# Optimization experiments

Hardware: AMD Instinct MI355X
Metric: run time of the kernel (lower is better)

## Reference

```python
import jax, jax.numpy as jnp
import numpy as np

N = 100000   # nodes
E = 1600000  # edges
G = 512      # graphs in batch
F_IN = 128
H = 128
F_OUT = 1


def setup_inputs() -> dict:
    key = jax.random.key(0)
    ks = jax.random.split(key, 12)
    x = jax.random.normal(ks[0], (N, F_IN), dtype=jnp.float32)
    src = jax.random.randint(ks[1], (E,), 0, N, dtype=jnp.int32)
    dst = jax.random.randint(ks[2], (E,), 0, N, dtype=jnp.int32)
    node2graph = jnp.sort(jax.random.randint(ks[3], (N,), 0, G, dtype=jnp.int32))
    s_in = 1.0 / np.sqrt(F_IN)
    s_h = 1.0 / np.sqrt(H)
    W0 = jax.random.normal(ks[4], (F_IN, H), dtype=jnp.float32) * s_in
    b0 = jnp.zeros((H,), dtype=jnp.float32)
    W1 = jax.random.normal(ks[5], (H, H), dtype=jnp.float32) * s_h
    b1 = jnp.zeros((H,), dtype=jnp.float32)
    W2 = jax.random.normal(ks[6], (H, H), dtype=jnp.float32) * s_h
    b2 = jnp.zeros((H,), dtype=jnp.float32)
    Wm1 = jax.random.normal(ks[7], (H, H), dtype=jnp.float32) * s_h
    bm1 = jnp.zeros((H,), dtype=jnp.float32)
    Wm2 = jax.random.normal(ks[8], (H, F_OUT), dtype=jnp.float32) * s_h
    bm2 = jnp.zeros((F_OUT,), dtype=jnp.float32)
    return {"x": x, "src": src, "dst": dst, "node2graph": node2graph,
            "W0": W0, "b0": b0, "W1": W1, "b1": b1, "W2": W2, "b2": b2,
            "Wm1": Wm1, "bm1": bm1, "Wm2": Wm2, "bm2": bm2}


def _degree_norms(src, dst):
    ones = jnp.ones((E,), dtype=jnp.float32)
    out_deg = jax.ops.segment_sum(ones, src, num_segments=N)
    in_deg = jax.ops.segment_sum(ones, dst, num_segments=N)
    norm_out = jax.lax.rsqrt(jnp.maximum(out_deg, 1.0))  # [N]
    norm_in = jax.lax.rsqrt(jnp.maximum(in_deg, 1.0))    # [N]
    return norm_out, norm_in


def _graph_conv(x, src, dst, norm_out, norm_in, W, b):
    # DGL GraphConv, norm='both', in_feats <= out_feats path:
    # aggregate normalized src features, then linear + activation.
    xs = x * norm_out[:, None]
    msg = xs[src]                                         # [E, H] gather
    agg = jax.ops.segment_sum(msg, dst, num_segments=N)   # [N, H] scatter-add
    agg = agg * norm_in[:, None]
    return jax.nn.relu(agg @ W + b)


def reference(x, src, dst, node2graph, W0, b0, W1, b1, W2, b2, Wm1, bm1, Wm2, bm2):
    norm_out, norm_in = _degree_norms(src, dst)
    h = _graph_conv(x, src, dst, norm_out, norm_in, W0, b0)
    h = _graph_conv(h, src, dst, norm_out, norm_in, W1, b1)
    h = _graph_conv(h, src, dst, norm_out, norm_in, W2, b2)
    # sum_nodes readout per graph
    g = jax.ops.segment_sum(h, node2graph, num_segments=G)  # [G, H]
    # MLP head: Linear -> ReLU -> Linear
    return jax.nn.relu(g @ Wm1 + bm1) @ Wm2 + bm2           # [G, 1]
```

## Files before the change

kernel.cpp:

```cpp
#include <hip/hip_runtime.h>

#define NN 100000
#define NE 1600000
#define NG 512
#define HD 128

#define NBK 196
#define CHUNK 6400
#define NC 250
#define LH (2 * NBK * NC)
#define BCAP 11264

typedef _Float16 h8 __attribute__((ext_vector_type(8)));
typedef float f32x4 __attribute__((ext_vector_type(4)));

__global__ __launch_bounds__(1024) void k_hist(const int* __restrict__ src,
                                               const int* __restrict__ dst,
                                               int* __restrict__ H,
                                               const float* __restrict__ W0,
                                               const float* __restrict__ W1,
                                               const float* __restrict__ W2,
                                               _Float16* __restrict__ Bt) {
    if (blockIdx.x >= NC) {
        int i = (blockIdx.x - NC) * 1024 + threadIdx.x;
        int w = i >> 14;
        int rem = i & 16383;
        int n = rem >> 7;
        int k = rem & 127;
        const float* W = (w == 0) ? W0 : ((w == 1) ? W1 : W2);
        Bt[i] = (_Float16)W[k * 128 + n];
        return;
    }
    __shared__ int hd[NBK], hs[NBK];
    int c = blockIdx.x;
    for (int i = threadIdx.x; i < NBK; i += 1024) { hd[i] = 0; hs[i] = 0; }
    __syncthreads();
    int e0 = c * CHUNK;
    int e1 = e0 + CHUNK; if (e1 > NE) e1 = NE;
    for (int e = e0 + threadIdx.x; e < e1; e += 1024) {
        atomicAdd(&hd[dst[e] >> 9], 1);
        atomicAdd(&hs[src[e] >> 9], 1);
    }
    __syncthreads();
    for (int i = threadIdx.x; i < NBK; i += 1024) {
        H[i * NC + c] = hd[i];
        H[NBK * NC + i * NC + c] = hs[i];
    }
}

__global__ __launch_bounds__(256) void k_scan1g(int* __restrict__ H,
                                                int* __restrict__ bsum, int L) {
    __shared__ int s[256];
    int i = blockIdx.x * 256 + threadIdx.x;
    int v = (i < L) ? H[i] : 0;
    s[threadIdx.x] = v;
    __syncthreads();
    for (int off = 1; off < 256; off <<= 1) {
        int t = (threadIdx.x >= off) ? s[threadIdx.x - off] : 0;
        __syncthreads();
        s[threadIdx.x] += t;
        __syncthreads();
    }
    if (i < L) H[i] = s[threadIdx.x] - v;
    if (threadIdx.x == 255) bsum[blockIdx.x] = s[255];
}

__global__ __launch_bounds__(256) void k_scan3g(int* __restrict__ H,
                                                const int* __restrict__ bsum,
                                                int L, int nb) {
    __shared__ int sb[512];
    __shared__ int tmp2[256];
    int t = threadIdx.x;
    int b0 = (2 * t < nb) ? bsum[2 * t] : 0;
    int b1 = (2 * t + 1 < nb) ? bsum[2 * t + 1] : 0;
    int pair = b0 + b1;
    tmp2[t] = pair;
    __syncthreads();
    for (int off = 1; off < 256; off <<= 1) {
        int v2 = (t >= off) ? tmp2[t - off] : 0;
        __syncthreads();
        tmp2[t] += v2;
        __syncthreads();
    }
    int ex = tmp2[t] - pair;
    sb[2 * t] = ex;
    sb[2 * t + 1] = ex + b0;
    __syncthreads();
    int i = blockIdx.x * 256 + t;
    if (i < L) H[i] += sb[i >> 8];
}

__global__ __launch_bounds__(1024) void k_scatter(const int* __restrict__ src,
                                                  const int* __restrict__ dst,
                                                  const int* __restrict__ H,
                                                  int* __restrict__ dpart,
                                                  unsigned short* __restrict__ spart) {
    __shared__ int valbuf[CHUNK];
    __shared__ unsigned short bidbuf[CHUNK];
    __shared__ int lcur[NBK], delta[NBK];
    __shared__ int tmp[256];
    int c = blockIdx.x;
    int t = threadIdx.x;
    int e0 = c * CHUNK;
    int e1 = e0 + CHUNK; if (e1 > NE) e1 = NE;
    int n = e1 - e0;

    {
        int v = 0;
        if (t < NBK) {
            int curp = H[t * NC + c];
            int nxtp = (c + 1 < NC) ? H[t * NC + c + 1]
                                    : ((t + 1 < NBK) ? H[(t + 1) * NC] : NE);
            v = nxtp - curp;
            delta[t] = curp;
        }
        if (t < 256) tmp[t] = v;
        __syncthreads();
        for (int off = 1; off < 256; off <<= 1) {
            int add = (t < 256 && t >= off) ? tmp[t - off] : 0;
            __syncthreads();
            if (t < 256) tmp[t] += add;
            __syncthreads();
        }
        if (t < NBK) {
            int lbase = tmp[t] - v;
            lcur[t] = lbase;
            delta[t] -= lbase;
        }
    }
    __syncthreads();
    for (int e = e0 + t; e < e1; e += 1024) {
        int s = src[e], d = dst[e];
        int b = d >> 9;
        int q = atomicAdd(&lcur[b], 1);
        valbuf[q] = s | ((d & 511) << 17);
        bidbuf[q] = (unsigned short)b;
    }
    __syncthreads();
    for (int i = t; i < n; i += 1024) dpart[delta[bidbuf[i]] + i] = valbuf[i];
    __syncthreads();

    {
        int v = 0;
        if (t < NBK) {
            int curp = H[NBK * NC + t * NC + c] - NE;
            int nxtp = (c + 1 < NC) ? H[NBK * NC + t * NC + c + 1] - NE
                                    : ((t + 1 < NBK) ? H[NBK * NC + (t + 1) * NC] - NE : NE);
            v = nxtp - curp;
            delta[t] = curp;
        }
        if (t < 256) tmp[t] = v;
        __syncthreads();
        for (int off = 1; off < 256; off <<= 1) {
            int add = (t < 256 && t >= off) ? tmp[t - off] : 0;
            __syncthreads();
            if (t < 256) tmp[t] += add;
            __syncthreads();
        }
        if (t < NBK) {
            int lbase = tmp[t] - v;
            lcur[t] = lbase;
            delta[t] -= lbase;
        }
    }
    __syncthreads();
    for (int e = e0 + t; e < e1; e += 1024) {
        int s = src[e];
        int b = s >> 9;
        int q = atomicAdd(&lcur[b], 1);
        valbuf[q] = s & 511;
        bidbuf[q] = (unsigned short)b;
    }
    __syncthreads();
    for (int i = t; i < n; i += 1024)
        spart[delta[bidbuf[i]] + i] = (unsigned short)valbuf[i];
}

__global__ __launch_bounds__(1024) void k_bucket(const int* __restrict__ dpart,
                                                 const unsigned short* __restrict__ spart,
                                                 const int* __restrict__ H,
                                                 int* __restrict__ offs,
                                                 int* __restrict__ csr,
                                                 float* __restrict__ ni,
                                                 float* __restrict__ no) {
    __shared__ int deg[512];
    __shared__ int lcur[512];
    __shared__ int tmp[1024];
    __shared__ int csrbuf[BCAP];
    int b = blockIdx.x;
    bool isDst = (b < NBK);
    int bb = isDst ? b : b - NBK;
    int start, end;
    if (isDst) {
        start = H[bb * NC];
        end = (bb + 1 < NBK) ? H[(bb + 1) * NC] : NE;
    } else {
        start = H[NBK * NC + bb * NC] - NE;
        end = (bb + 1 < NBK) ? H[NBK * NC + (bb + 1) * NC] - NE : NE;
    }
    int t = threadIdx.x;
    if (t < 512) deg[t] = 0;
    __syncthreads();
    if (isDst) {
        for (int i = start + t; i < end; i += 1024)
            atomicAdd(&deg[(dpart[i] >> 17) & 511], 1);
    } else {
        for (int i = start + t; i < end; i += 1024)
            atomicAdd(&deg[spart[i]], 1);
    }
    __syncthreads();
    int vb = bb * 512;
    if (!isDst) {
        if (t < 512) {
            int v = vb + t;
            if (v < NN) no[v] = rsqrtf(fmaxf((float)deg[t], 1.0f));
        }
        return;
    }
    int a = (t < 512) ? deg[t] : 0;
    tmp[t] = a;
    __syncthreads();
    for (int off = 1; off < 1024; off <<= 1) {
        int v2 = (t >= off) ? tmp[t - off] : 0;
        __syncthreads();
        tmp[t] += v2;
        __syncthreads();
    }
    if (t < 512) {
        lcur[t] = tmp[t] - a;
        int v = vb + t;
        if (v < NN) {
            offs[v] = start + lcur[t];
            ni[v] = rsqrtf(fmaxf((float)a, 1.0f));
        }
    }
    if (b == NBK - 1 && t == 0) offs[NN] = NE;
    __syncthreads();
    int len = end - start;
    bool fits = (len <= BCAP);
    for (int i = start + t; i < end; i += 1024) {
        int pk = dpart[i];
        int q = atomicAdd(&lcur[(pk >> 17) & 511], 1);
        if (fits) csrbuf[q] = pk & 0x1FFFF;
        else      csr[start + q] = pk & 0x1FFFF;
    }
    __syncthreads();
    if (fits) {
        for (int i = t; i < len; i += 1024) csr[start + i] = csrbuf[i];
    }
}

template <typename TA>
__global__ __launch_bounds__(256) void k_gemm_mfma(const TA* __restrict__ A,
                                                   const _Float16* __restrict__ Bt,
                                                   const float* __restrict__ no,
                                                   _Float16* __restrict__ Zh,
                                                   int nrows) {
    __shared__ _Float16 Bs[128 * 136];
    int tid = threadIdx.x;
    {
        const h8* B8 = (const h8*)Bt;
        h8* Bs8 = (h8*)Bs;
        for (int i = tid; i < 2048; i += 256) {
            int n = i >> 4, c = i & 15;
            Bs8[n * 17 + c] = B8[i];
        }
    }

    int wave = tid >> 6;
    int lane = tid & 63;
    int m16 = lane & 15;
    int quad = lane >> 4;
    int rowbase = blockIdx.x * 64 + wave * 16;
    int row = rowbase + m16;
    bool valid = row < nrows;

    h8 afrag[4];
    if (valid) {
        if constexpr (sizeof(TA) == 2) {
            const h8* Arow = (const h8*)(A + (size_t)row * 128);
#pragma unroll
            for (int kk = 0; kk < 4; kk++) afrag[kk] = Arow[kk * 4 + quad];
        } else {
            const float4* Arow = (const float4*)(A + (size_t)row * 128);
#pragma unroll
            for (int kk = 0; kk < 4; kk++) {
                float4 lo = Arow[kk * 8 + quad * 2];
                float4 hi = Arow[kk * 8 + quad * 2 + 1];
                h8 a;
                a[0] = (_Float16)lo.x; a[1] = (_Float16)lo.y;
                a[2] = (_Float16)lo.z; a[3] = (_Float16)lo.w;
                a[4] = (_Float16)hi.x; a[5] = (_Float16)hi.y;
                a[6] = (_Float16)hi.z; a[7] = (_Float16)hi.w;
                afrag[kk] = a;
            }
        }
    } else {
#pragma unroll
        for (int kk = 0; kk < 4; kk++) {
            h8 a;
#pragma unroll
            for (int j = 0; j < 8; j++) a[j] = (_Float16)0.f;
            afrag[kk] = a;
        }
    }

    __syncthreads();

    f32x4 acc[8];
#pragma unroll
    for (int nt = 0; nt < 8; nt++) acc[nt] = (f32x4){0.f, 0.f, 0.f, 0.f};

    const h8* Bs8 = (const h8*)Bs;
#pragma unroll
    for (int nt = 0; nt < 8; nt++) {
        const h8* Bp = Bs8 + (size_t)(nt * 16 + m16) * 17;
#pragma unroll
        for (int kk = 0; kk < 4; kk++) {
            acc[nt] = __builtin_amdgcn_mfma_f32_16x16x32_f16(afrag[kk], Bp[kk * 4 + quad],
                                                             acc[nt], 0, 0, 0);
        }
    }

    float nor[4];
#pragma unroll
    for (int r = 0; r < 4; r++) {
        int grow = rowbase + quad * 4 + r;
        nor[r] = (grow < nrows) ? no[grow] : 0.f;
    }

    __syncthreads();
    {
        int lr0 = wave * 16 + quad * 4;
#pragma unroll
        for (int nt = 0; nt < 8; nt++) {
#pragma unroll
            for (int r = 0; r < 4; r++) {
                Bs[(size_t)(lr0 + r) * 136 + nt * 16 + m16] =
                    (_Float16)(acc[nt][r] * nor[r]);
            }
        }
    }
    __syncthreads();

    int blockrow0 = blockIdx.x * 64;
    for (int i = tid; i < 1024; i += 256) {
        int r = i >> 4, cch = i & 15;
        int grow = blockrow0 + r;
        if (grow < nrows) {
            h8 val = *(const h8*)&Bs[(size_t)r * 136 + cch * 8];
            *(h8*)&Zh[(size_t)grow * 128 + cch * 8] = val;
        }
    }
}

__global__ __launch_bounds__(256) void k_agg(const h8* __restrict__ Zh,
                                             const int* __restrict__ offs,
                                             const int* __restrict__ csr,
                                             const float* __restrict__ ni,
                                             const float* __restrict__ b,
                                             h8* __restrict__ H16) {
    int v = blockIdx.x * 16 + (threadIdx.x >> 4);
    int c = threadIdx.x & 15;
    int s = offs[v];
    int e = offs[v + 1];
    float a0[8], a1[8];
#pragma unroll
    for (int j = 0; j < 8; j++) { a0[j] = 0.f; a1[j] = 0.f; }
    int i = s;
    for (; i + 4 <= e; i += 4) {
        int u0 = csr[i];
        int u1 = csr[i + 1];
        int u2 = csr[i + 2];
        int u3 = csr[i + 3];
        h8 z0 = Zh[(size_t)u0 * 16 + c];
        h8 z1 = Zh[(size_t)u1 * 16 + c];
        h8 z2 = Zh[(size_t)u2 * 16 + c];
        h8 z3 = Zh[(size_t)u3 * 16 + c];
#pragma unroll
        for (int j = 0; j < 8; j++) {
            a0[j] += (float)z0[j] + (float)z1[j];
            a1[j] += (float)z2[j] + (float)z3[j];
        }
    }
    for (; i < e; i++) {
        int u = csr[i];
        h8 z = Zh[(size_t)u * 16 + c];
#pragma unroll
        for (int j = 0; j < 8; j++) a0[j] += (float)z[j];
    }
    float niv = ni[v];
    const float* bb = b + c * 8;
    h8 r;
#pragma unroll
    for (int j = 0; j < 8; j++)
        r[j] = (_Float16)fmaxf((a0[j] + a1[j]) * niv + bb[j], 0.f);
    H16[(size_t)v * 16 + c] = r;
}

__global__ __launch_bounds__(256) void k_gsum(const h8* __restrict__ H8,
                                              const int* __restrict__ n2g,
                                              float* __restrict__ gbuf) {
    __shared__ float red[256 * 8];
    int gi = blockIdx.x >> 2;
    int part = blockIdx.x & 3;
    int t = threadIdx.x;
    int slot = t >> 4;
    int c = t & 15;

    int lo = 0, hi = NN;
    while (lo < hi) { int mid = (lo + hi) >> 1; if (n2g[mid] < gi) lo = mid + 1; else hi = mid; }
    int s = lo;
    hi = NN;
    while (lo < hi) { int mid = (lo + hi) >> 1; if (n2g[mid] < gi + 1) lo = mid + 1; else hi = mid; }
    int e = lo;

    float acc[8];
#pragma unroll
    for (int j = 0; j < 8; j++) acc[j] = 0.f;
    for (int v = s + part * 16 + slot; v < e; v += 64) {
        h8 z = H8[(size_t)v * 16 + c];
#pragma unroll
        for (int j = 0; j < 8; j++) acc[j] += (float)z[j];
    }
#pragma unroll
    for (int j = 0; j < 8; j++) red[t * 8 + j] = acc[j];
    __syncthreads();
    for (int off = 8; off >= 1; off >>= 1) {
        if (slot < off) {
#pragma unroll
            for (int j = 0; j < 8; j++)
                red[t * 8 + j] += red[(t + off * 16) * 8 + j];
        }
        __syncthreads();
    }
    if (slot == 0) {
#pragma unroll
        for (int j = 0; j < 8; j++)
            gbuf[((size_t)part * NG + gi) * 128 + c * 8 + j] = red[t * 8 + j];
    }
}

__global__ __launch_bounds__(128) void k_head(const float* __restrict__ gbuf,
                                              const float* __restrict__ Wm1,
                                              const float* __restrict__ bm1,
                                              const float* __restrict__ Wm2,
                                              const float* __restrict__ bm2,
                                              float* __restrict__ out) {
    __shared__ float gs[128];
    __shared__ float red2[128];
    int gi = blockIdx.x;
    int t = threadIdx.x;
    gs[t] = gbuf[(size_t)gi * 128 + t] +
            gbuf[((size_t)NG + gi) * 128 + t] +
            gbuf[((size_t)2 * NG + gi) * 128 + t] +
            gbuf[((size_t)3 * NG + gi) * 128 + t];
    __syncthreads();
    float a = bm1[t];
    for (int k = 0; k < 128; k++) a += gs[k] * Wm1[k * 128 + t];
    red2[t] = fmaxf(a, 0.f) * Wm2[t];
    __syncthreads();
    for (int s2 = 64; s2 > 0; s2 >>= 1) {
        if (t < s2) red2[t] += red2[t + s2];
        __syncthreads();
    }
    if (t == 0) out[gi] = red2[0] + bm2[0];
}

extern "C" void kernel_launch(void* const* d_in, const int* in_sizes, int n_in,
                              void* d_out, int out_size, void* d_ws, size_t ws_size,
                              hipStream_t stream) {
    const float* x   = (const float*)d_in[0];
    const int*   src = (const int*)d_in[1];
    const int*   dst = (const int*)d_in[2];
    const int*   n2g = (const int*)d_in[3];
    const float* W0  = (const float*)d_in[4];
    const float* b0  = (const float*)d_in[5];
    const float* W1  = (const float*)d_in[6];
    const float* b1  = (const float*)d_in[7];
    const float* W2  = (const float*)d_in[8];
    const float* b2  = (const float*)d_in[9];
    const float* Wm1 = (const float*)d_in[10];
    const float* bm1 = (const float*)d_in[11];
    const float* Wm2 = (const float*)d_in[12];
    const float* bm2 = (const float*)d_in[13];
    float* out = (float*)d_out;

    char* p = (char*)d_ws;
    auto carve = [&](size_t bytes) -> char* {
        char* r = p;
        p += (bytes + 255) & ~(size_t)255;
        return r;
    };
    _Float16* zh  = (_Float16*)carve((size_t)NN * HD * 2);
    _Float16* h16 = (_Float16*)carve((size_t)NN * HD * 2);
    _Float16* Bt  = (_Float16*)carve((size_t)3 * 128 * 128 * 2);
    float* no     = (float*)carve((size_t)NN * 4);
    float* ni     = (float*)carve((size_t)NN * 4);
    int*   offs   = (int*)carve((size_t)(NN + 1) * 4);
    int*   csr    = (int*)carve((size_t)NE * 4);
    int*   Hh     = (int*)carve((size_t)LH * 4);
    int*   bsum   = (int*)carve((size_t)512 * 4);
    int*   dpart  = (int*)carve((size_t)NE * 4);
    unsigned short* spart = (unsigned short*)carve((size_t)NE * 2);
    float* gbuf   = (float*)carve((size_t)4 * NG * 128 * 4);

    int scan_blocks = (LH + 255) / 256;
    k_hist<<<NC + 48, 1024, 0, stream>>>(src, dst, Hh, W0, W1, W2, Bt);
    k_scan1g<<<scan_blocks, 256, 0, stream>>>(Hh, bsum, LH);
    k_scan3g<<<scan_blocks, 256, 0, stream>>>(Hh, bsum, LH, scan_blocks);
    k_scatter<<<NC, 1024, 0, stream>>>(src, dst, Hh, dpart, spart);
    k_bucket<<<2 * NBK, 1024, 0, stream>>>(dpart, spart, Hh, offs, csr, ni, no);

    int gemm_blocks = (NN + 63) / 64;
    int agg_blocks  = NN / 16;

    k_gemm_mfma<float><<<gemm_blocks, 256, 0, stream>>>(x, Bt, no, zh, NN);
    k_agg<<<agg_blocks, 256, 0, stream>>>((const h8*)zh, offs, csr, ni, b0, (h8*)h16);
    k_gemm_mfma<_Float16><<<gemm_blocks, 256, 0, stream>>>(h16, Bt + 16384, no, zh, NN);
    k_agg<<<agg_blocks, 256, 0, stream>>>((const h8*)zh, offs, csr, ni, b1, (h8*)h16);
    k_gemm_mfma<_Float16><<<gemm_blocks, 256, 0, stream>>>(h16, Bt + 32768, no, zh, NN);
    k_agg<<<agg_blocks, 256, 0, stream>>>((const h8*)zh, offs, csr, ni, b2, (h8*)h16);

    k_gsum<<<NG * 4, 256, 0, stream>>>((const h8*)h16, n2g, gbuf);
    k_head<<<NG, 128, 0, stream>>>(gbuf, Wm1, bm1, Wm2, bm2, out);
}
```

Before: 372.0 us.

## Fuse CSR build pipeline into one cooperative kernel with grid syncs

```diff
diff --git a/kernel.cpp b/kernel.cpp
--- a/kernel.cpp
+++ b/kernel.cpp
@@ -1,4 +1,7 @@
 #include <hip/hip_runtime.h>
+#include <hip/hip_cooperative_groups.h>
+
+namespace cg = cooperative_groups;
 
 #define NN 100000
 #define NE 1600000
@@ -9,111 +12,70 @@
 #define CHUNK 6400
 #define NC 250
 #define LH (2 * NBK * NC)
+#define SLICE 392
 #define BCAP 11264
 
 typedef _Float16 h8 __attribute__((ext_vector_type(8)));
 typedef float f32x4 __attribute__((ext_vector_type(4)));
 
-__global__ __launch_bounds__(1024) void k_hist(const int* __restrict__ src,
-                                               const int* __restrict__ dst,
-                                               int* __restrict__ H,
-                                               const float* __restrict__ W0,
-                                               const float* __restrict__ W1,
-                                               const float* __restrict__ W2,
-                                               _Float16* __restrict__ Bt) {
-    if (blockIdx.x >= NC) {
-        int i = (blockIdx.x - NC) * 1024 + threadIdx.x;
-        int w = i >> 14;
-        int rem = i & 16383;
-        int n = rem >> 7;
-        int k = rem & 127;
-        const float* W = (w == 0) ? W0 : ((w == 1) ? W1 : W2);
-        Bt[i] = (_Float16)W[k * 128 + n];
-        return;
-    }
-    __shared__ int hd[NBK], hs[NBK];
-    int c = blockIdx.x;
-    for (int i = threadIdx.x; i < NBK; i += 1024) { hd[i] = 0; hs[i] = 0; }
-    __syncthreads();
-    int e0 = c * CHUNK;
-    int e1 = e0 + CHUNK; if (e1 > NE) e1 = NE;
-    for (int e = e0 + threadIdx.x; e < e1; e += 1024) {
-        atomicAdd(&hd[dst[e] >> 9], 1);
-        atomicAdd(&hs[src[e] >> 9], 1);
-    }
-    __syncthreads();
-    for (int i = threadIdx.x; i < NBK; i += 1024) {
-        H[i * NC + c] = hd[i];
-        H[NBK * NC + i * NC + c] = hs[i];
-    }
-}
-
-__global__ __launch_bounds__(256) void k_scan1g(int* __restrict__ H,
-                                                int* __restrict__ bsum, int L) {
-    __shared__ int s[256];
-    int i = blockIdx.x * 256 + threadIdx.x;
-    int v = (i < L) ? H[i] : 0;
-    s[threadIdx.x] = v;
-    __syncthreads();
-    for (int off = 1; off < 256; off <<= 1) {
-        int t = (threadIdx.x >= off) ? s[threadIdx.x - off] : 0;
-        __syncthreads();
-        s[threadIdx.x] += t;
-        __syncthreads();
-    }
-    if (i < L) H[i] = s[threadIdx.x] - v;
-    if (threadIdx.x == 255) bsum[blockIdx.x] = s[255];
-}
-
-__global__ __launch_bounds__(256) void k_scan3g(int* __restrict__ H,
-                                                const int* __restrict__ bsum,
-                                                int L, int nb) {
-    __shared__ int sb[512];
-    __shared__ int tmp2[256];
+__global__ __launch_bounds__(1024, 1) void k_build(
+    const int* __restrict__ src, const int* __restrict__ dst,
+    int* __restrict__ H, int* __restrict__ ssum,
+    int* __restrict__ dpart, unsigned short* __restrict__ spart,
+    int* __restrict__ offs, int* __restrict__ csr,
+    float* __restrict__ ni, float* __restrict__ no,
+    const float* __restrict__ W0, const float* __restrict__ W1,
+    const float* __restrict__ W2, _Float16* __restrict__ Bt) {
+    cg::grid_group grid = cg::this_grid();
+    __shared__ __align__(16) char smem[54848];
+    int* sl = (int*)smem;
+    char* scratch = smem + 1600;
+    int bid = blockIdx.x;
     int t = threadIdx.x;
-    int b0 = (2 * t < nb) ? bsum[2 * t] : 0;
-    int b1 = (2 * t + 1 < nb) ? bsum[2 * t + 1] : 0;
-    int pair = b0 + b1;
-    tmp2[t] = pair;
-    __syncthreads();
-    for (int off = 1; off < 256; off <<= 1) {
-        int v2 = (t >= off) ? tmp2[t - off] : 0;
-        __syncthreads();
-        tmp2[t] += v2;
-        __syncthreads();
-    }
-    int ex = tmp2[t] - pair;
-    sb[2 * t] = ex;
-    sb[2 * t + 1] = ex + b0;
-    __syncthreads();
-    int i = blockIdx.x * 256 + t;
-    if (i < L) H[i] += sb[i >> 8];
-}
-
-__global__ __launch_bounds__(1024) void k_scatter(const int* __restrict__ src,
-                                                  const int* __restrict__ dst,
-                                                  const int* __restrict__ H,
-                                                  int* __restrict__ dpart,
-                                                  unsigned short* __restrict__ spart) {
-    __shared__ int valbuf[CHUNK];
-    __shared__ unsigned short bidbuf[CHUNK];
-    __shared__ int lcur[NBK], delta[NBK];
-    __shared__ int tmp[256];
-    int c = blockIdx.x;
-    int t = threadIdx.x;
-    int e0 = c * CHUNK;
-    int e1 = e0 + CHUNK; if (e1 > NE) e1 = NE;
-    int n = e1 - e0;
-
-    {
-        int v = 0;
+
+    {
+        int* hd = (int*)scratch;
+        int* hs = hd + NBK;
+        if (t < NBK) { hd[t] = 0; hs[t] = 0; }
+        __syncthreads();
+        int e0 = bid * CHUNK;
+        for (int e = e0 + t; e < e0 + CHUNK; e += 1024) {
+            atomicAdd(&hd[dst[e] >> 9], 1);
+            atomicAdd(&hs[src[e] >> 9], 1);
+        }
+        for (int i = bid * 1024 + t; i < 3 * 16384; i += NC * 1024) {
+            int w = i >> 14, rem = i & 16383;
+            int n = rem >> 7, k = rem & 127;
+            const float* W = (w == 0) ? W0 : ((w == 1) ? W1 : W2);
+            Bt[i] = (_Float16)W[k * 128 + n];
+        }
+        __syncthreads();
         if (t < NBK) {
-            int curp = H[t * NC + c];
-            int nxtp = (c + 1 < NC) ? H[t * NC + c + 1]
-                                    : ((t + 1 < NBK) ? H[(t + 1) * NC] : NE);
-            v = nxtp - curp;
-            delta[t] = curp;
-        }
+            H[t * NC + bid] = hd[t];
+            H[NBK * NC + t * NC + bid] = hs[t];
+        }
+    }
+    grid.sync();
+
+    {
+        int* tmp = (int*)scratch;
+        int v = (t < SLICE) ? H[bid * SLICE + t] : 0;
+        if (t < 512) tmp[t] = v;
+        __syncthreads();
+        for (int off = 1; off < 512; off <<= 1) {
+            int add = (t < 512 && t >= off) ? tmp[t - off] : 0;
+            __syncthreads();
+            if (t < 512) tmp[t] += add;
+            __syncthreads();
+        }
+        if (t < SLICE) sl[t] = tmp[t] - v;
+        if (t == 511) ssum[bid] = tmp[511];
+    }
+    grid.sync();
+
+    if (bid == 0) {
+        int* tmp = (int*)scratch;
+        int v = (t < NC) ? ssum[t] : 0;
         if (t < 256) tmp[t] = v;
         __syncthreads();
         for (int off = 1; off < 256; off <<= 1) {
@@ -122,131 +84,166 @@
             if (t < 256) tmp[t] += add;
             __syncthreads();
         }
-        if (t < NBK) {
-            int lbase = tmp[t] - v;
-            lcur[t] = lbase;
-            delta[t] -= lbase;
-        }
-    }
-    __syncthreads();
-    for (int e = e0 + t; e < e1; e += 1024) {
-        int s = src[e], d = dst[e];
-        int b = d >> 9;
-        int q = atomicAdd(&lcur[b], 1);
-        valbuf[q] = s | ((d & 511) << 17);
-        bidbuf[q] = (unsigned short)b;
-    }
-    __syncthreads();
-    for (int i = t; i < n; i += 1024) dpart[delta[bidbuf[i]] + i] = valbuf[i];
-    __syncthreads();
-
-    {
-        int v = 0;
-        if (t < NBK) {
-            int curp = H[NBK * NC + t * NC + c] - NE;
-            int nxtp = (c + 1 < NC) ? H[NBK * NC + t * NC + c + 1] - NE
-                                    : ((t + 1 < NBK) ? H[NBK * NC + (t + 1) * NC] - NE : NE);
-            v = nxtp - curp;
-            delta[t] = curp;
-        }
-        if (t < 256) tmp[t] = v;
-        __syncthreads();
-        for (int off = 1; off < 256; off <<= 1) {
-            int add = (t < 256 && t >= off) ? tmp[t - off] : 0;
-            __syncthreads();
-            if (t < 256) tmp[t] += add;
-            __syncthreads();
-        }
-        if (t < NBK) {
-            int lbase = tmp[t] - v;
-            lcur[t] = lbase;
-            delta[t] -= lbase;
-        }
-    }
-    __syncthreads();
-    for (int e = e0 + t; e < e1; e += 1024) {
-        int s = src[e];
-        int b = s >> 9;
-        int q = atomicAdd(&lcur[b], 1);
-        valbuf[q] = s & 511;
-        bidbuf[q] = (unsigned short)b;
-    }
-    __syncthreads();
-    for (int i = t; i < n; i += 1024)
-        spart[delta[bidbuf[i]] + i] = (unsigned short)valbuf[i];
-}
-
-__global__ __launch_bounds__(1024) void k_bucket(const int* __restrict__ dpart,
-                                                 const unsigned short* __restrict__ spart,
-                                                 const int* __restrict__ H,
-                                                 int* __restrict__ offs,
-                                                 int* __restrict__ csr,
-                                                 float* __restrict__ ni,
-                                                 float* __restrict__ no) {
-    __shared__ int deg[512];
-    __shared__ int lcur[512];
-    __shared__ int tmp[1024];
-    __shared__ int csrbuf[BCAP];
-    int b = blockIdx.x;
-    bool isDst = (b < NBK);
-    int bb = isDst ? b : b - NBK;
-    int start, end;
-    if (isDst) {
-        start = H[bb * NC];
-        end = (bb + 1 < NBK) ? H[(bb + 1) * NC] : NE;
-    } else {
-        start = H[NBK * NC + bb * NC] - NE;
-        end = (bb + 1 < NBK) ? H[NBK * NC + (bb + 1) * NC] - NE : NE;
-    }
-    int t = threadIdx.x;
-    if (t < 512) deg[t] = 0;
-    __syncthreads();
-    if (isDst) {
-        for (int i = start + t; i < end; i += 1024)
-            atomicAdd(&deg[(dpart[i] >> 17) & 511], 1);
-    } else {
-        for (int i = start + t; i < end; i += 1024)
-            atomicAdd(&deg[spart[i]], 1);
-    }
-    __syncthreads();
-    int vb = bb * 512;
-    if (!isDst) {
-        if (t < 512) {
-            int v = vb + t;
-            if (v < NN) no[v] = rsqrtf(fmaxf((float)deg[t], 1.0f));
-        }
-        return;
-    }
-    int a = (t < 512) ? deg[t] : 0;
-    tmp[t] = a;
-    __syncthreads();
-    for (int off = 1; off < 1024; off <<= 1) {
-        int v2 = (t >= off) ? tmp[t - off] : 0;
-        __syncthreads();
-        tmp[t] += v2;
-        __syncthreads();
-    }
-    if (t < 512) {
-        lcur[t] = tmp[t] - a;
-        int v = vb + t;
-        if (v < NN) {
-            offs[v] = start + lcur[t];
-            ni[v] = rsqrtf(fmaxf((float)a, 1.0f));
-        }
-    }
-    if (b == NBK - 1 && t == 0) offs[NN] = NE;
-    __syncthreads();
-    int len = end - start;
-    bool fits = (len <= BCAP);
-    for (int i = start + t; i < end; i += 1024) {
-        int pk = dpart[i];
-        int q = atomicAdd(&lcur[(pk >> 17) & 511], 1);
-        if (fits) csrbuf[q] = pk & 0x1FFFF;
-        else      csr[start + q] = pk & 0x1FFFF;
-    }
-    __syncthreads();
-    if (fits) {
-        for (int i = t; i < len; i += 1024) csr[start + i] = csrbuf[i];
+        if (t < NC) ssum[t] = tmp[t] - v;
+    }
+    grid.sync();
+
+    {
+        int p = ssum[bid];
+        if (t < SLICE) H[bid * SLICE + t] = sl[t] + p;
+    }
+    grid.sync();
+
+    {
+        int* valbuf = (int*)scratch;
+        unsigned short* bidbuf = (unsigned short*)(scratch + 25600);
+        int* lcur = (int*)(scratch + 38400);
+        int* delta = (int*)(scratch + 39184);
+        int* tmp = (int*)(scratch + 39968);
+        int c = bid;
+        int e0 = c * CHUNK;
+        int e1 = e0 + CHUNK;
+
+        {
+            int v = 0;
+            if (t < NBK) {
+                int curp = H[t * NC + c];
+                int nxtp = (c + 1 < NC) ? H[t * NC + c + 1]
+                                        : ((t + 1 < NBK) ? H[(t + 1) * NC] : NE);
+                v = nxtp - curp;
+                delta[t] = curp;
+            }
+            if (t < 256) tmp[t] = v;
+            __syncthreads();
+            for (int off = 1; off < 256; off <<= 1) {
+                int add = (t < 256 && t >= off) ? tmp[t - off] : 0;
+                __syncthreads();
+                if (t < 256) tmp[t] += add;
+                __syncthreads();
+            }
+            if (t < NBK) {
+                int lbase = tmp[t] - v;
+                lcur[t] = lbase;
+                delta[t] -= lbase;
+            }
+        }
+        __syncthreads();
+        for (int e = e0 + t; e < e1; e += 1024) {
+            int s = src[e], d = dst[e];
+            int b = d >> 9;
+            int q = atomicAdd(&lcur[b], 1);
+            valbuf[q] = s | ((d & 511) << 17);
+            bidbuf[q] = (unsigned short)b;
+        }
+        __syncthreads();
+        for (int i = t; i < CHUNK; i += 1024) dpart[delta[bidbuf[i]] + i] = valbuf[i];
+        __syncthreads();
+
+        {
+            int v = 0;
+            if (t < NBK) {
+                int curp = H[NBK * NC + t * NC + c] - NE;
+                int nxtp = (c + 1 < NC) ? H[NBK * NC + t * NC + c + 1] - NE
+                                        : ((t + 1 < NBK) ? H[NBK * NC + (t + 1) * NC] - NE : NE);
+                v = nxtp - curp;
+                delta[t] = curp;
+            }
+            if (t < 256) tmp[t] = v;
+            __syncthreads();
+            for (int off = 1; off < 256; off <<= 1) {
+                int add = (t < 256 && t >= off) ? tmp[t - off] : 0;
+                __syncthreads();
+                if (t < 256) tmp[t] += add;
+                __syncthreads();
+            }
+            if (t < NBK) {
+                int lbase = tmp[t] - v;
+                lcur[t] = lbase;
+                delta[t] -= lbase;
+            }
+        }
+        __syncthreads();
+        for (int e = e0 + t; e < e1; e += 1024) {
+            int s = src[e];
+            int b = s >> 9;
+            int q = atomicAdd(&lcur[b], 1);
+            valbuf[q] = s & 511;
+            bidbuf[q] = (unsigned short)b;
+        }
+        __syncthreads();
+        for (int i = t; i < CHUNK; i += 1024)
+            spart[delta[bidbuf[i]] + i] = (unsigned short)valbuf[i];
+    }
+    grid.sync();
+
+    {
+        int* deg = (int*)scratch;
+        int* lcur = (int*)(scratch + 2048);
+        int* tmp = (int*)(scratch + 4096);
+        int* csrbuf = (int*)(scratch + 8192);
+        for (int task = bid; task < 2 * NBK; task += NC) {
+            bool isDst = (task < NBK);
+            int bb = isDst ? task : task - NBK;
+            int start, end;
+            if (isDst) {
+                start = H[bb * NC];
+                end = (bb + 1 < NBK) ? H[(bb + 1) * NC] : NE;
+            } else {
+                start = H[NBK * NC + bb * NC] - NE;
+                end = (bb + 1 < NBK) ? H[NBK * NC + (bb + 1) * NC] - NE : NE;
+            }
+            if (t < 512) deg[t] = 0;
+            __syncthreads();
+            if (isDst) {
+                for (int i = start + t; i < end; i += 1024)
+                    atomicAdd(&deg[(dpart[i] >> 17) & 511], 1);
+            } else {
+                for (int i = start + t; i < end; i += 1024)
+                    atomicAdd(&deg[spart[i]], 1);
+            }
+            __syncthreads();
+            int vb = bb * 512;
+            if (!isDst) {
+                if (t < 512) {
+                    int v = vb + t;
+                    if (v < NN) no[v] = rsqrtf(fmaxf((float)deg[t], 1.0f));
+                }
+                __syncthreads();
+                continue;
+            }
+            int a = (t < 512) ? deg[t] : 0;
+            tmp[t] = a;
+            __syncthreads();
+            for (int off = 1; off < 1024; off <<= 1) {
+                int v2 = (t >= off) ? tmp[t - off] : 0;
+                __syncthreads();
+                tmp[t] += v2;
+                __syncthreads();
+            }
+            if (t < 512) {
+                lcur[t] = tmp[t] - a;
+                int v = vb + t;
+                if (v < NN) {
+                    offs[v] = start + lcur[t];
+                    ni[v] = rsqrtf(fmaxf((float)a, 1.0f));
+                }
+            }
+            if (task == NBK - 1 && t == 0) offs[NN] = NE;
+            __syncthreads();
+            int len = end - start;
+            bool fits = (len <= BCAP);
+            for (int i = start + t; i < end; i += 1024) {
+                int pk = dpart[i];
+                int q = atomicAdd(&lcur[(pk >> 17) & 511], 1);
+                if (fits) csrbuf[q] = pk & 0x1FFFF;
+                else      csr[start + q] = pk & 0x1FFFF;
+            }
+            __syncthreads();
+            if (fits) {
+                for (int i = t; i < len; i += 1024) csr[start + i] = csrbuf[i];
+            }
+            __syncthreads();
+        }
     }
 }
 
@@ -500,17 +497,19 @@
     int*   offs   = (int*)carve((size_t)(NN + 1) * 4);
     int*   csr    = (int*)carve((size_t)NE * 4);
     int*   Hh     = (int*)carve((size_t)LH * 4);
-    int*   bsum   = (int*)carve((size_t)512 * 4);
+    int*   ssum   = (int*)carve((size_t)512 * 4);
     int*   dpart  = (int*)carve((size_t)NE * 4);
     unsigned short* spart = (unsigned short*)carve((size_t)NE * 2);
     float* gbuf   = (float*)carve((size_t)4 * NG * 128 * 4);
 
-    int scan_blocks = (LH + 255) / 256;
-    k_hist<<<NC + 48, 1024, 0, stream>>>(src, dst, Hh, W0, W1, W2, Bt);
-    k_scan1g<<<scan_blocks, 256, 0, stream>>>(Hh, bsum, LH);
-    k_scan3g<<<scan_blocks, 256, 0, stream>>>(Hh, bsum, LH, scan_blocks);
-    k_scatter<<<NC, 1024, 0, stream>>>(src, dst, Hh, dpart, spart);
-    k_bucket<<<2 * NBK, 1024, 0, stream>>>(dpart, spart, Hh, offs, csr, ni, no);
+    {
+        void* args[] = {(void*)&src, (void*)&dst, (void*)&Hh, (void*)&ssum,
+                        (void*)&dpart, (void*)&spart, (void*)&offs, (void*)&csr,
+                        (void*)&ni, (void*)&no, (void*)&W0, (void*)&W1,
+                        (void*)&W2, (void*)&Bt};
+        hipLaunchCooperativeKernel((const void*)k_build, dim3(NC), dim3(1024),
+                                   args, 0, stream);
+    }
 
     int gemm_blocks = (NN + 63) / 64;
     int agg_blocks  = NN / 16;
```

Result: slower. 539.0 us (+44.9%).
